# Performance work log

Measured on AMD Instinct MI355X. Metric: run time of the kernel, lower is better.

Reference implementation:

```python
import jax, jax.numpy as jnp
import numpy as np

HEAD = 4
EPS = 1e-12


def _l2norm(x, axis):
    # torch F.normalize: x / max(||x||_2, eps)
    return x / jnp.maximum(jnp.linalg.norm(x, axis=axis, keepdims=True), EPS)


def setup_inputs() -> dict:
    key = jax.random.key(0)
    ks = jax.random.split(key, 12)
    n, t, c, h, w = 2, 7, 96, 96, 96
    inp = {
        "curr_feat": jax.random.normal(ks[0], (n, c, h, w), jnp.float32),
        "index_feat_set_s1": jax.random.normal(ks[1], (n, t, c, h, w), jnp.float32),
        "anchor_feat": jax.random.normal(ks[2], (n, c, h, w), jnp.float32),
        "sparse_feat_set_s1": jax.random.normal(ks[3], (n, t, c, h, w), jnp.float32),
        "sparse_feat_set_s2": jax.random.normal(ks[4], (n, t, c, h, w), jnp.float32),
        "sparse_feat_set_s3": jax.random.normal(ks[5], (n, t, c, h, w), jnp.float32),
        # absolute pixel coordinates (x,y interleaved per frame), mostly in-bounds
        # with a little overshoot to exercise zeros padding of grid_sample
        "location_feat": jax.random.uniform(ks[6], (n, t * 2, h, w), jnp.float32, minval=-2.0, maxval=float(w) + 1.0),
        "proj_w": 0.02 * jax.random.normal(ks[7], (c, c), jnp.float32),
        "proj_b": jnp.zeros((c,), jnp.float32),
        "fusion_w": 0.02 * jax.random.normal(ks[8], (c, 3 * c), jnp.float32),
        "fusion_b": jnp.zeros((c,), jnp.float32),
    }
    return inp


def reference(curr_feat, index_feat_set_s1, anchor_feat, sparse_feat_set_s1,
              sparse_feat_set_s2, sparse_feat_set_s3, location_feat,
              proj_w, proj_b, fusion_w, fusion_b):
    n, c, h, w = anchor_feat.shape
    t = sparse_feat_set_s1.shape[1]
    hd = c // HEAD
    hw = h * w

    # ---- flow-guided nearest grid_sample (align_corners=True, zeros pad) ----
    loc = location_feat.reshape(n, t, 2, h, w)  # (n,t,2,h,w): [x, y] pixel coords
    gx = 2.0 * loc[:, :, 0] / max(w - 1, 1) - 1.0
    gy = 2.0 * loc[:, :, 1] / max(h - 1, 1) - 1.0
    ix = jnp.round((gx + 1.0) * 0.5 * (w - 1))  # nearest (round-half-even, as torch)
    iy = jnp.round((gy + 1.0) * 0.5 * (h - 1))
    valid = (ix >= 0) & (ix <= w - 1) & (iy >= 0) & (iy <= h - 1)
    lin = (jnp.clip(iy, 0, h - 1).astype(jnp.int32) * w
           + jnp.clip(ix, 0, w - 1).astype(jnp.int32)).reshape(n, t, 1, hw)
    vmask = valid.reshape(n, t, 1, hw)

    def sample(f):  # f: (n,t,c,h,w) -> gathered (n,t,c,hw)
        g = jnp.take_along_axis(f.reshape(n, t, c, hw), lin, axis=3)
        return jnp.where(vmask, g, 0.0)

    samp1 = sample(sparse_feat_set_s1)
    samp2 = sample(sparse_feat_set_s2)
    samp3 = sample(sparse_feat_set_s3)
    sampi = sample(index_feat_set_s1)

    # ---- per-pixel multi-head max-correlation over t frames ----
    # queries: normalize over full channel dim c BEFORE splitting into heads
    q = _l2norm(curr_feat.reshape(n, c, hw).transpose(0, 2, 1), -1).reshape(n, hw, HEAD, hd)
    k = _l2norm(sampi.transpose(0, 3, 1, 2), -1).reshape(n, hw, t, HEAD, hd)
    scores = jnp.einsum('npthd,nphd->npht', k, q)  # scale == 1.0 in mode='max'
    corr_soft = jnp.max(scores, axis=3)     # (n,hw,head)
    corr_index = jnp.argmax(scores, axis=3)  # (n,hw,head), first-max like torch

    soft_img = jnp.broadcast_to(corr_soft[..., None], (n, hw, HEAD, hd)) \
                  .reshape(n, h, w, c).transpose(0, 3, 1, 2)  # (n,c,h,w)
    idx = jnp.broadcast_to(corr_index[..., None], (n, hw, HEAD, hd)) \
             .reshape(n, hw, c).transpose(0, 2, 1)[:, None]  # (n,1,c,hw)

    def pick(samp):  # select winning frame per (channel-group, pixel)
        return jnp.take_along_axis(samp, idx, axis=1)[:, 0].reshape(n, c, h, w)

    cat = jnp.concatenate([pick(samp1), pick(samp2), pick(samp3)], axis=1)  # (n,3c,h,w)
    out = jnp.einsum('ndhw,cd->nchw', cat, fusion_w) + fusion_b[None, :, None, None]
    out = out * soft_img
    out = jnp.einsum('nchw,dc->ndhw', out, proj_w) + proj_b[None, :, None, None]
    return out + anchor_feat
```

## Files before the change

kernel.cpp:

```cpp
#include <hip/hip_runtime.h>
#include <hip/hip_bf16.h>

#define N_    2
#define T_    7
#define C_    96
#define H_    96
#define W_    96
#define HW_   9216
#define HEAD_ 4
#define HD_   24
#define C3_   288
#define P_    16
#define QP_   100
#define CATP_ 292
#define NBLK_ (N_ * (HW_ / P_))
#define PLANES_ 14
#define CHUNK_  48
#define NCHUNK_ 192
#define TBLK_ (PLANES_ * NCHUNK_)

typedef unsigned int u32;

__device__ __forceinline__ float bits2f(u32 b) {
    union { u32 u; float f; } x; x.u = b; return x.f;
}

__device__ __forceinline__ unsigned short f2bf(float f) {
    union { __hip_bfloat16 h; unsigned short s; } u;
    u.h = __float2bfloat16(f);
    return u.s;
}

template<bool BF16>
__device__ __forceinline__ float ld1(const void* p, int i) {
    if constexpr (BF16) return bits2f(((u32)((const unsigned short*)p)[i]) << 16);
    else                return ((const float*)p)[i];
}

template<bool BF16>
__device__ __forceinline__ void ld4w(const void* p, int i, float w[4]) {
    if constexpr (BF16) {
        const uint2 u = ((const uint2*)p)[i >> 2];
        w[0] = bits2f(u.x << 16);
        w[1] = bits2f(u.x & 0xFFFF0000u);
        w[2] = bits2f(u.y << 16);
        w[3] = bits2f(u.y & 0xFFFF0000u);
    } else {
        const float4 v = *((const float4*)((const float*)p + i));
        w[0] = v.x; w[1] = v.y; w[2] = v.z; w[3] = v.w;
    }
}

template<bool BF16>
__device__ __forceinline__ void st1(void* p, int i, float v) {
    if constexpr (BF16) ((unsigned short*)p)[i] = f2bf(v);
    else                ((float*)p)[i] = v;
}

template<bool BF16>
__device__ __forceinline__ void st4w(void* p, int i, const float v[4]) {
    if constexpr (BF16) {
        uint2 w;
        w.x = (u32)f2bf(v[0]) | ((u32)f2bf(v[1]) << 16);
        w.y = (u32)f2bf(v[2]) | ((u32)f2bf(v[3]) << 16);
        ((uint2*)p)[i >> 2] = w;
    } else {
        *((float4*)((float*)p + i)) = make_float4(v[0], v[1], v[2], v[3]);
    }
}

__device__ __forceinline__ bool block_detect_bf16(const u32* __restrict__ w,
                                                  int tid, int* s_flag) {
    if (tid < 64) {
        u32 x = w[tid];
        u32 f = x & 0x7FFFu;
        int inwin = (f >= 0x3A00u) && (f <= 0x4200u);
        unsigned long long m = __ballot(inwin);
        if (tid == 0) *s_flag = (__popcll(m) >= 40) ? 1 : 0;
    }
    __syncthreads();
    return *s_flag != 0;
}

template<bool BF16>
__device__ __forceinline__ void transp_swz(const void* __restrict__ src,
                                           void* __restrict__ dst,
                                           int pl, int x0, int tid, char* raw) {
    if constexpr (BF16) {
        unsigned short* tile = (unsigned short*)raw;
        const unsigned short* s = (const unsigned short*)src;
        unsigned short* d = (unsigned short*)dst;
        for (int i = tid; i < C_ * (CHUNK_ / 4); i += 256) {
            int ch = i / 12, xq = i - ch * 12;
            const ushort4 v = *((const ushort4*)(s + (pl * C_ + ch) * HW_ + x0 + 4 * xq));
            int g = (ch >> 2) ^ (xq & 7);
            int chl = ch & 3;
            tile[(4 * xq + 0) * 96 + 4 * g + chl] = v.x;
            tile[(4 * xq + 1) * 96 + 4 * g + chl] = v.y;
            tile[(4 * xq + 2) * 96 + 4 * g + chl] = v.z;
            tile[(4 * xq + 3) * 96 + 4 * g + chl] = v.w;
        }
        __syncthreads();
        for (int i = tid; i < CHUNK_ * (C_ / 4); i += 256) {
            int p = i / 24, cq = i - p * 24;
            int g = cq ^ ((p >> 2) & 7);
            const ushort4 v = *((const ushort4*)&tile[p * 96 + 4 * g]);
            *((ushort4*)(d + (pl * HW_ + x0 + p) * C_ + 4 * cq)) = v;
        }
    } else {
        float* tile = (float*)raw;
        const float* s = (const float*)src;
        float* d = (float*)dst;
        for (int i = tid; i < C_ * (CHUNK_ / 4); i += 256) {
            int ch = i / 12, xq = i - ch * 12;
            const float4 v = *((const float4*)(s + (pl * C_ + ch) * HW_ + x0 + 4 * xq));
            int g = (ch >> 2) ^ (xq & 7);
            int chl = ch & 3;
            tile[(4 * xq + 0) * 96 + 4 * g + chl] = v.x;
            tile[(4 * xq + 1) * 96 + 4 * g + chl] = v.y;
            tile[(4 * xq + 2) * 96 + 4 * g + chl] = v.z;
            tile[(4 * xq + 3) * 96 + 4 * g + chl] = v.w;
        }
        __syncthreads();
        for (int i = tid; i < CHUNK_ * (C_ / 4); i += 256) {
            int p = i / 24, cq = i - p * 24;
            int g = cq ^ ((p >> 2) & 7);
            const float4 v = *((const float4*)&tile[p * 96 + 4 * g]);
            *((float4*)(d + (pl * HW_ + x0 + p) * C_ + 4 * cq)) = v;
        }
    }
}

__global__ __launch_bounds__(256) void transp_kernel(
    const void* __restrict__ a0, const void* __restrict__ a1,
    const void* __restrict__ a2, const void* __restrict__ a3,
    void* __restrict__ dstb, unsigned long long szb,
    const u32* __restrict__ detect_src)
{
    __shared__ __align__(16) char raw[CHUNK_ * 96 * 4];
    __shared__ int s_flag;
    const int arr = blockIdx.y;
    const void* src = (arr == 0) ? a0 : (arr == 1) ? a1 : (arr == 2) ? a2 : a3;
    void* dst = (char*)dstb + (unsigned long long)arr * szb;
    const int tid = threadIdx.x;
    const int pl = blockIdx.x / NCHUNK_;
    const int x0 = (blockIdx.x - pl * NCHUNK_) * CHUNK_;
    const bool bf = block_detect_bf16(detect_src, tid, &s_flag);
    if (bf) transp_swz<true >(src, dst, pl, x0, tid, raw);
    else    transp_swz<false>(src, dst, pl, x0, tid, raw);
}

template<bool BF16, bool TGB>
__device__ __forceinline__ void argmax_body(
    const void* __restrict__ curr, const void* __restrict__ loc,
    const void* __restrict__ kT,
    float* __restrict__ ws_best, int* __restrict__ ws_gbase,
    float* s_u, int (*s_lin)[P_], float (*s_red)[8],
    float (*s_best)[HEAD_], int (*s_bidx)[HEAD_], float* s_inv)
{
#define S_Q(pp, ch)  s_u[(pp) * QP_ + (ch)]
#define S_K(pp, ch)  s_u[P_ * QP_ + (pp) * QP_ + (ch)]
    const int tid = threadIdx.x;
    const int b  = blockIdx.x;
    const int nn = b / (HW_ / P_);
    const int p0 = (b - nn * (HW_ / P_)) * P_;

    if (tid < T_ * P_) {
        int t = tid / P_, pp = tid - t * P_;
        int p = p0 + pp;
        float x = ld1<BF16>(loc, (nn * 2 * T_ + 2 * t    ) * HW_ + p);
        float y = ld1<BF16>(loc, (nn * 2 * T_ + 2 * t + 1) * HW_ + p);
        float gx = 2.0f * x / 95.0f - 1.0f;
        float gy = 2.0f * y / 95.0f - 1.0f;
        float fx = (gx + 1.0f) * 0.5f * 95.0f;
        float fy = (gy + 1.0f) * 0.5f * 95.0f;
        float ix = rintf(fx), iy = rintf(fy);
        bool v = (ix >= 0.0f) && (ix <= 95.0f) && (iy >= 0.0f) && (iy <= 95.0f);
        s_lin[t][pp] = v ? ((int)iy * W_ + (int)ix) : -1;
    }
    if (tid >= 128 && tid < 128 + P_ * HEAD_) {
        int q = tid - 128;
        s_best[q >> 2][q & 3] = -3.0e38f; s_bidx[q >> 2][q & 3] = 0;
    }

    for (int i = tid; i < C_ * (P_ / 4); i += 256) {
        int ch = i >> 2, pq = i & 3;
        float w[4];
        ld4w<BF16>(curr, (nn * C_ + ch) * HW_ + p0 + 4 * pq, w);
        S_Q(4 * pq + 0, ch) = w[0]; S_Q(4 * pq + 1, ch) = w[1];
        S_Q(4 * pq + 2, ch) = w[2]; S_Q(4 * pq + 3, ch) = w[3];
    }
    __syncthreads();

    if (tid < P_ * 8) {
        int pp = tid >> 3, j = tid & 7;
        float s = 0.f;
        #pragma unroll
        for (int k = 0; k < 12; ++k) { float v = S_Q(pp, j * 12 + k); s += v * v; }
        s_red[pp][j] = s;
    }
    __syncthreads();
    if (tid < P_) {
        float s = 0.f;
        #pragma unroll
        for (int j = 0; j < 8; ++j) s += s_red[tid][j];
        s_inv[tid] = 1.0f / fmaxf(sqrtf(s), 1e-12f);
    }
    __syncthreads();
    for (int i = tid; i < C_ * P_; i += 256) {
        int pp = i & (P_ - 1), ch = i >> 4;
        S_Q(pp, ch) *= s_inv[pp];
    }

    const int pp0 = tid / 24,        j0 = tid - pp0 * 24;
    const int pp1 = (tid + 256) / 24, j1 = (tid + 256) - pp1 * 24;
    const bool has1 = (tid < 128);

    float4 ka0, ka1;
    {
        int lin = s_lin[0][pp0];
        float w[4] = {0.f, 0.f, 0.f, 0.f};
        if (lin >= 0) ld4w<BF16>(kT, ((nn * T_) * HW_ + lin) * C_ + 4 * j0, w);
        ka0 = make_float4(w[0], w[1], w[2], w[3]);
        if (has1) {
            int lin2 = s_lin[0][pp1];
            float w2[4] = {0.f, 0.f, 0.f, 0.f};
            if (lin2 >= 0) ld4w<BF16>(kT, ((nn * T_) * HW_ + lin2) * C_ + 4 * j1, w2);
            ka1 = make_float4(w2[0], w2[1], w2[2], w2[3]);
        }
    }

    for (int t = 0; t < T_; ++t) {
        __syncthreads();
        *((float4*)&S_K(pp0, 4 * j0)) = ka0;
        if (has1) *((float4*)&S_K(pp1, 4 * j1)) = ka1;
        if (t + 1 < T_) {
            int lin = s_lin[t + 1][pp0];
            float w[4] = {0.f, 0.f, 0.f, 0.f};
            if (lin >= 0) ld4w<BF16>(kT, ((nn * T_ + t + 1) * HW_ + lin) * C_ + 4 * j0, w);
            ka0 = make_float4(w[0], w[1], w[2], w[3]);
            if (has1) {
                int lin2 = s_lin[t + 1][pp1];
                float w2[4] = {0.f, 0.f, 0.f, 0.f};
                if (lin2 >= 0) ld4w<BF16>(kT, ((nn * T_ + t + 1) * HW_ + lin2) * C_ + 4 * j1, w2);
                ka1 = make_float4(w2[0], w2[1], w2[2], w2[3]);
            }
        }
        __syncthreads();
        if (tid < P_ * 8) {
            int pp = tid >> 3, j = tid & 7;
            float s = 0.f;
            #pragma unroll
            for (int k = 0; k < 12; ++k) { float v = S_K(pp, j * 12 + k); s += v * v; }
            s_red[pp][j] = s;
        }
        __syncthreads();
        if (tid < P_) {
            float s = 0.f;
            #pragma unroll
            for (int j = 0; j < 8; ++j) s += s_red[tid][j];
            s_inv[tid] = 1.0f / fmaxf(sqrtf(s), 1e-12f);
        }
        __syncthreads();
        if (tid < P_ * HEAD_) {
            int pp = tid >> 2, h = tid & 3;
            float s = 0.f;
            #pragma unroll
            for (int dq = 0; dq < 6; ++dq) {
                const float4 kv = *((const float4*)&S_K(pp, h * HD_ + 4 * dq));
                const float4 qv = *((const float4*)&S_Q(pp, h * HD_ + 4 * dq));
                s += kv.x * qv.x; s += kv.y * qv.y; s += kv.z * qv.z; s += kv.w * qv.w;
            }
            s *= s_inv[pp];
            if (s > s_best[pp][h]) { s_best[pp][h] = s; s_bidx[pp][h] = t; }
        }
    }
    if (tid < P_ * HEAD_) {
        int pp = tid >> 2, h = tid & 3;
        int bt = s_bidx[pp][h];
        int lin = s_lin[bt][pp];
        int g = (nn * HW_ + p0 + pp) * HEAD_ + h;
        ws_best[g] = s_best[pp][h];
        int gb;
        if (lin < 0)       gb = -1;
        else if (TGB)      gb = ((nn * T_ + bt) * HW_ + lin) * C_;
        else               gb = (nn * T_ + bt) * C_ * HW_ + lin;
        ws_gbase[g] = gb;
    }
#undef S_Q
#undef S_K
}

template<bool TGB>
__global__ __launch_bounds__(256, 8) void argmax_kernel(
    const void* __restrict__ curr, const void* __restrict__ loc,
    const void* __restrict__ kT,
    float* __restrict__ ws_best, int* __restrict__ ws_gbase)
{
    __shared__ __align__(16) float s_u[2 * P_ * QP_];
    __shared__ int   s_lin[T_][P_];
    __shared__ float s_red[P_][8];
    __shared__ float s_best[P_][HEAD_];
    __shared__ int   s_bidx[P_][HEAD_];
    __shared__ float s_inv[P_];
    __shared__ int   s_flag;
    const bool bf = block_detect_bf16((const u32*)curr, threadIdx.x, &s_flag);
    if (bf) argmax_body<true , TGB>(curr, loc, kT, ws_best, ws_gbase, s_u, s_lin, s_red, s_best, s_bidx, s_inv);
    else    argmax_body<false, TGB>(curr, loc, kT, ws_best, ws_gbase, s_u, s_lin, s_red, s_best, s_bidx, s_inv);
}

__global__ __launch_bounds__(256, 8) void fused_kernel(
    const void* __restrict__ curr, const void* __restrict__ loc,
    const void* __restrict__ kT,
    const void* __restrict__ s1, const void* __restrict__ s2,
    const void* __restrict__ s3,
    void* __restrict__ s123T, unsigned long long szb,
    float* __restrict__ ws_best, int* __restrict__ ws_gbase)
{
    __shared__ __align__(16) char raw[CHUNK_ * 96 * 4];
    __shared__ int s_flag;
    const int tid = threadIdx.x;
    const bool bf = block_detect_bf16((const u32*)curr, tid, &s_flag);
    const int bx = blockIdx.x;
    if (bx < NBLK_) {
        float* s_u            = (float*)raw;
        int   (*s_lin)[P_]    = (int(*)[P_])   (raw + 12800);
        float (*s_red)[8]     = (float(*)[8])  (raw + 13248);
        float (*s_best)[HEAD_]= (float(*)[HEAD_])(raw + 13760);
        int   (*s_bidx)[HEAD_]= (int(*)[HEAD_]) (raw + 14016);
        float* s_inv          = (float*)(raw + 14272);
        if (bf) argmax_body<true , true>(curr, loc, kT, ws_best, ws_gbase,
                                         s_u, s_lin, s_red, s_best, s_bidx, s_inv);
        else    argmax_body<false, true>(curr, loc, kT, ws_best, ws_gbase,
                                         s_u, s_lin, s_red, s_best, s_bidx, s_inv);
    } else {
        int t = bx - NBLK_;
        int arr = t / TBLK_;
        int bxx = t - arr * TBLK_;
        const void* src = (arr == 0) ? s1 : (arr == 1) ? s2 : s3;
        void* dst = (char*)s123T + (unsigned long long)arr * szb;
        int pl = bxx / NCHUNK_;
        int x0 = (bxx - pl * NCHUNK_) * CHUNK_;
        if (bf) transp_swz<true >(src, dst, pl, x0, tid, raw);
        else    transp_swz<false>(src, dst, pl, x0, tid, raw);
    }
}

template<bool BF16, bool TRANS>
__device__ __forceinline__ void catgemv_body(
    const void* __restrict__ anchor, const void* __restrict__ s1,
    const void* __restrict__ s2, const void* __restrict__ s3,
    const void* __restrict__ pw, const void* __restrict__ pb,
    const void* __restrict__ fw, const void* __restrict__ fb,
    void* __restrict__ outp,
    const float* __restrict__ ws_best, const int* __restrict__ ws_gbase,
    float* s_u, float (*s_mid)[QP_], float (*s_best)[HEAD_], int (*s_gbase)[HEAD_])
{
#define S_CAT(pp, d) s_u[(pp) * CATP_ + (d)]
    const int tid = threadIdx.x;
    const int b  = blockIdx.x;
    const int nn = b / (HW_ / P_);
    const int p0 = (b - nn * (HW_ / P_)) * P_;

    if (tid < P_ * HEAD_) {
        int pp = tid >> 2, h = tid & 3;
        int g = (nn * HW_ + p0 + pp) * HEAD_ + h;
        s_best[pp][h]  = ws_best[g];
        s_gbase[pp][h] = ws_gbase[g];
    }
    __syncthreads();

    if constexpr (TRANS) {
        for (int i = tid; i < P_ * 72; i += 256) {
            int px = i / 72, j = i - px * 72;
            int set = j / 24, jj = j - set * 24;
            int gb = s_gbase[px][jj / 6];
            float w[4] = {0.f, 0.f, 0.f, 0.f};
            if (gb >= 0) {
                const void* sp = (set == 0) ? s1 : (set == 1) ? s2 : s3;
                ld4w<BF16>(sp, gb + 4 * jj, w);
            }
            *((float4*)&S_CAT(px, set * C_ + 4 * jj)) = make_float4(w[0], w[1], w[2], w[3]);
        }
    } else {
        for (int i = tid; i < C3_ * P_; i += 256) {
            int pp = i / C3_, d = i - pp * C3_;
            int set = d / C_, ch = d - set * C_;
            int gb = s_gbase[pp][ch / HD_];
            float v = 0.f;
            if (gb >= 0) {
                const void* sp = (set == 0) ? s1 : (set == 1) ? s2 : s3;
                v = ld1<BF16>(sp, gb + ch * HW_);
            }
            S_CAT(pp, d) = v;
        }
    }
    __syncthreads();

    if (tid < 192) {
        const int cp = tid >> 2, pq = tid & 3;
        const int co0 = cp * 2, px0 = pq * 4;
        float acc[2][4];
        #pragma unroll
        for (int r = 0; r < 2; ++r)
            #pragma unroll
            for (int k = 0; k < 4; ++k) acc[r][k] = 0.f;
        for (int d = 0; d < C3_; d += 4) {
            float4 cv[4];
            #pragma unroll
            for (int k = 0; k < 4; ++k) cv[k] = *((const float4*)&S_CAT(px0 + k, d));
            #pragma unroll
            for (int r = 0; r < 2; ++r) {
                float w[4]; ld4w<BF16>(fw, (co0 + r) * C3_ + d, w);
                #pragma unroll
                for (int k = 0; k < 4; ++k)
                    acc[r][k] += w[0] * cv[k].x + w[1] * cv[k].y + w[2] * cv[k].z + w[3] * cv[k].w;
            }
        }
        const int hh = co0 / HD_;
        #pragma unroll
        for (int r = 0; r < 2; ++r) {
            float fbv = ld1<BF16>(fb, co0 + r);
            #pragma unroll
            for (int k = 0; k < 4; ++k)
                s_mid[px0 + k][co0 + r] = (acc[r][k] + fbv) * s_best[px0 + k][hh];
        }
    }
    __syncthreads();

    if (tid < 192) {
        const int dp = tid >> 2, pq = tid & 3;
        const int do0 = dp * 2, px0 = pq * 4;
        float acc[2][4];
        #pragma unroll
        for (int r = 0; r < 2; ++r)
            #pragma unroll
            for (int k = 0; k < 4; ++k) acc[r][k] = 0.f;
        for (int c = 0; c < C_; c += 4) {
            float4 mv[4];
            #pragma unroll
            for (int k = 0; k < 4; ++k) mv[k] = *((const float4*)&s_mid[px0 + k][c]);
            #pragma unroll
            for (int r = 0; r < 2; ++r) {
                float w[4]; ld4w<BF16>(pw, (do0 + r) * C_ + c, w);
                #pragma unroll
                for (int k = 0; k < 4; ++k)
                    acc[r][k] += w[0] * mv[k].x + w[1] * mv[k].y + w[2] * mv[k].z + w[3] * mv[k].w;
            }
        }
        #pragma unroll
        for (int r = 0; r < 2; ++r) {
            float pbv = ld1<BF16>(pb, do0 + r);
            float av[4];
            ld4w<BF16>(anchor, (nn * C_ + do0 + r) * HW_ + p0 + px0, av);
            float res[4];
            #pragma unroll
            for (int k = 0; k < 4; ++k) res[k] = acc[r][k] + pbv + av[k];
            st4w<BF16>(outp, (nn * C_ + do0 + r) * HW_ + p0 + px0, res);
        }
    }
#undef S_CAT
}

template<bool TRANS>
__global__ __launch_bounds__(256, 6) void catgemv_kernel(
    const void* __restrict__ curr, const void* __restrict__ anchor,
    const void* __restrict__ s1, const void* __restrict__ s2,
    const void* __restrict__ s3, const void* __restrict__ pw,
    const void* __restrict__ pb, const void* __restrict__ fw,
    const void* __restrict__ fb, void* __restrict__ outp,
    const float* __restrict__ ws_best, const int* __restrict__ ws_gbase)
{
    __shared__ __align__(16) float s_u[P_ * CATP_];
    __shared__ __align__(16) float s_mid[P_][QP_];
    __shared__ float s_best[P_][HEAD_];
    __shared__ int   s_gbase[P_][HEAD_];
    __shared__ int   s_flag;
    const bool bf = block_detect_bf16((const u32*)curr, threadIdx.x, &s_flag);
    if (bf) catgemv_body<true , TRANS>(anchor, s1, s2, s3, pw, pb, fw, fb, outp, ws_best, ws_gbase,
                                       s_u, s_mid, s_best, s_gbase);
    else    catgemv_body<false, TRANS>(anchor, s1, s2, s3, pw, pb, fw, fb, outp, ws_best, ws_gbase,
                                       s_u, s_mid, s_best, s_gbase);
}

template<bool BF16>
__device__ __forceinline__ void mono_body(
    const void* __restrict__ curr, const void* __restrict__ idxf,
    const void* __restrict__ anchor, const void* __restrict__ s1,
    const void* __restrict__ s2, const void* __restrict__ s3,
    const void* __restrict__ loc, const void* __restrict__ pw,
    const void* __restrict__ pb, const void* __restrict__ fw,
    const void* __restrict__ fb, void* __restrict__ outp,
    float* s_u, float (*s_mid)[QP_], int (*s_lin)[P_], float (*s_red)[8],
    float (*s_best)[HEAD_], int (*s_bidx)[HEAD_], float* s_inv)
{
#define S_Q(pp, ch)  s_u[(pp) * QP_ + (ch)]
#define S_K(pp, ch)  s_u[P_ * QP_ + (pp) * QP_ + (ch)]
#define S_CAT(pp, d) s_u[(pp) * CATP_ + (d)]
    const int tid = threadIdx.x;
    const int b  = blockIdx.x;
    const int nn = b / (HW_ / P_);
    const int p0 = (b - nn * (HW_ / P_)) * P_;

    if (tid < T_ * P_) {
        int t = tid / P_, pp = tid - t * P_;
        int p = p0 + pp;
        float x = ld1<BF16>(loc, (nn * 2 * T_ + 2 * t    ) * HW_ + p);
        float y = ld1<BF16>(loc, (nn * 2 * T_ + 2 * t + 1) * HW_ + p);
        float gx = 2.0f * x / 95.0f - 1.0f;
        float gy = 2.0f * y / 95.0f - 1.0f;
        float fx = (gx + 1.0f) * 0.5f * 95.0f;
        float fy = (gy + 1.0f) * 0.5f * 95.0f;
        float ix = rintf(fx), iy = rintf(fy);
        bool v = (ix >= 0.0f) && (ix <= 95.0f) && (iy >= 0.0f) && (iy <= 95.0f);
        s_lin[t][pp] = v ? ((int)iy * W_ + (int)ix) : -1;
    }
    if (tid >= 128 && tid < 128 + P_ * HEAD_) {
        int q = tid - 128;
        s_best[q >> 2][q & 3] = -3.0e38f; s_bidx[q >> 2][q & 3] = 0;
    }
    for (int i = tid; i < C_ * (P_ / 4); i += 256) {
        int ch = i >> 2, pq = i & 3;
        float w[4];
        ld4w<BF16>(curr, (nn * C_ + ch) * HW_ + p0 + 4 * pq, w);
        S_Q(4 * pq + 0, ch) = w[0]; S_Q(4 * pq + 1, ch) = w[1];
        S_Q(4 * pq + 2, ch) = w[2]; S_Q(4 * pq + 3, ch) = w[3];
    }
    __syncthreads();
    if (tid < P_ * 8) {
        int pp = tid >> 3, j = tid & 7;
        float s = 0.f;
        #pragma unroll
        for (int k = 0; k < 12; ++k) { float v = S_Q(pp, j * 12 + k); s += v * v; }
        s_red[pp][j] = s;
    }
    __syncthreads();
    if (tid < P_) {
        float s = 0.f;
        #pragma unroll
        for (int j = 0; j < 8; ++j) s += s_red[tid][j];
        s_inv[tid] = 1.0f / fmaxf(sqrtf(s), 1e-12f);
    }
    __syncthreads();
    for (int i = tid; i < C_ * P_; i += 256) {
        int pp = i & (P_ - 1), ch = i >> 4;
        S_Q(pp, ch) *= s_inv[pp];
    }
    for (int t = 0; t < T_; ++t) {
        __syncthreads();
        for (int i = tid; i < C_ * P_; i += 256) {
            int ch = i / P_, pp = i - ch * P_;
            int lin = s_lin[t][pp];
            S_K(pp, ch) = (lin >= 0) ? ld1<BF16>(idxf, ((nn * T_ + t) * C_ + ch) * HW_ + lin) : 0.0f;
        }
        __syncthreads();
        if (tid < P_ * 8) {
            int pp = tid >> 3, j = tid & 7;
            float s = 0.f;
            #pragma unroll
            for (int k = 0; k < 12; ++k) { float v = S_K(pp, j * 12 + k); s += v * v; }
            s_red[pp][j] = s;
        }
        __syncthreads();
        if (tid < P_) {
            float s = 0.f;
            #pragma unroll
            for (int j = 0; j < 8; ++j) s += s_red[tid][j];
            s_inv[tid] = 1.0f / fmaxf(sqrtf(s), 1e-12f);
        }
        __syncthreads();
        if (tid < P_ * HEAD_) {
            int pp = tid >> 2, h = tid & 3;
            float s = 0.f;
            #pragma unroll
            for (int dq = 0; dq < 6; ++dq) {
                const float4 kv = *((const float4*)&S_K(pp, h * HD_ + 4 * dq));
                const float4 qv = *((const float4*)&S_Q(pp, h * HD_ + 4 * dq));
                s += kv.x * qv.x; s += kv.y * qv.y; s += kv.z * qv.z; s += kv.w * qv.w;
            }
            s *= s_inv[pp];
            if (s > s_best[pp][h]) { s_best[pp][h] = s; s_bidx[pp][h] = t; }
        }
    }
    __syncthreads();
    for (int i = tid; i < C3_ * P_; i += 256) {
        int pp = i / C3_, d = i - pp * C3_;
        int set = d / C_, ch = d - set * C_;
        int h = ch / HD_;
        int bt = s_bidx[pp][h];
        int lin = s_lin[bt][pp];
        float v = 0.f;
        if (lin >= 0) {
            const void* sp = (set == 0) ? s1 : (set == 1) ? s2 : s3;
            v = ld1<BF16>(sp, ((nn * T_ + bt) * C_ + ch) * HW_ + lin);
        }
        S_CAT(pp, d) = v;
    }
    __syncthreads();
    if (tid < 96) {
        const int cq = tid >> 2, pq = tid & 3;
        const int co0 = cq * 4, px0 = pq * 4;
        float acc[4][4];
        #pragma unroll
        for (int r = 0; r < 4; ++r)
            #pragma unroll
            for (int k = 0; k < 4; ++k) acc[r][k] = 0.f;
        for (int d = 0; d < C3_; d += 4) {
            float4 cv[4];
            #pragma unroll
            for (int k = 0; k < 4; ++k) cv[k] = *((const float4*)&S_CAT(px0 + k, d));
            #pragma unroll
            for (int r = 0; r < 4; ++r) {
                float w[4]; ld4w<BF16>(fw, (co0 + r) * C3_ + d, w);
                #pragma unroll
                for (int k = 0; k < 4; ++k)
                    acc[r][k] += w[0] * cv[k].x + w[1] * cv[k].y + w[2] * cv[k].z + w[3] * cv[k].w;
            }
        }
        const int hh = co0 / HD_;
        #pragma unroll
        for (int r = 0; r < 4; ++r) {
            float fbv = ld1<BF16>(fb, co0 + r);
            #pragma unroll
            for (int k = 0; k < 4; ++k)
                s_mid[px0 + k][co0 + r] = (acc[r][k] + fbv) * s_best[px0 + k][hh];
        }
    }
    __syncthreads();
    if (tid < 96) {
        const int dq = tid >> 2, pq = tid & 3;
        const int do0 = dq * 4, px0 = pq * 4;
        float acc[4][4];
        #pragma unroll
        for (int r = 0; r < 4; ++r)
            #pragma unroll
            for (int k = 0; k < 4; ++k) acc[r][k] = 0.f;
        for (int c = 0; c < C_; c += 4) {
            float4 mv[4];
            #pragma unroll
            for (int k = 0; k < 4; ++k) mv[k] = *((const float4*)&s_mid[px0 + k][c]);
            #pragma unroll
            for (int r = 0; r < 4; ++r) {
                float w[4]; ld4w<BF16>(pw, (do0 + r) * C_ + c, w);
                #pragma unroll
                for (int k = 0; k < 4; ++k)
                    acc[r][k] += w[0] * mv[k].x + w[1] * mv[k].y + w[2] * mv[k].z + w[3] * mv[k].w;
            }
        }
        #pragma unroll
        for (int r = 0; r < 4; ++r) {
            float pbv = ld1<BF16>(pb, do0 + r);
            float av[4];
            ld4w<BF16>(anchor, (nn * C_ + do0 + r) * HW_ + p0 + px0, av);
            float res[4];
            #pragma unroll
            for (int k = 0; k < 4; ++k) res[k] = acc[r][k] + pbv + av[k];
            st4w<BF16>(outp, (nn * C_ + do0 + r) * HW_ + p0 + px0, res);
        }
    }
#undef S_Q
#undef S_K
#undef S_CAT
}

__global__ __launch_bounds__(256) void mono_kernel(
    const void* __restrict__ curr, const void* __restrict__ idxf,
    const void* __restrict__ anchor, const void* __restrict__ s1,
    const void* __restrict__ s2, const void* __restrict__ s3,
    const void* __restrict__ loc, const void* __restrict__ pw,
    const void* __restrict__ pb, const void* __restrict__ fw,
    const void* __restrict__ fb, void* __restrict__ outp)
{
    __shared__ __align__(16) float s_u[P_ * CATP_];
    __shared__ __align__(16) float s_mid[P_][QP_];
    __shared__ int   s_lin[T_][P_];
    __shared__ float s_red[P_][8];
    __shared__ float s_best[P_][HEAD_];
    __shared__ int   s_bidx[P_][HEAD_];
    __shared__ float s_inv[P_];
    __shared__ int   s_flag;
    const bool bf = block_detect_bf16((const u32*)curr, threadIdx.x, &s_flag);
    if (bf) mono_body<true >(curr, idxf, anchor, s1, s2, s3, loc, pw, pb, fw, fb, outp,
                             s_u, s_mid, s_lin, s_red, s_best, s_bidx, s_inv);
    else    mono_body<false>(curr, idxf, anchor, s1, s2, s3, loc, pw, pb, fw, fb, outp,
                             s_u, s_mid, s_lin, s_red, s_best, s_bidx, s_inv);
}

extern "C" void kernel_launch(void* const* d_in, const int* in_sizes, int n_in,
                              void* d_out, int out_size, void* d_ws, size_t ws_size,
                              hipStream_t stream) {
    (void)in_sizes; (void)n_in; (void)out_size;
    const unsigned long long SZB  = (unsigned long long)N_ * T_ * HW_ * C_ * 4ull;
    const unsigned long long AUXB = (unsigned long long)N_ * HW_ * HEAD_ * 4ull;
    char* wsb = (char*)d_ws;

    dim3 grid(NBLK_), block(256);
    if (ws_size >= 4 * SZB + 2 * AUXB) {
        void*  kT       = wsb;
        void*  s123T    = wsb + SZB;
        float* ws_best  = (float*)(wsb + 4 * SZB);
        int*   ws_gbase = (int*)  (wsb + 4 * SZB + AUXB);
        transp_kernel<<<dim3(TBLK_, 1), 256, 0, stream>>>(
            d_in[1], d_in[1], d_in[1], d_in[1], kT, SZB, (const u32*)d_in[0]);
        fused_kernel<<<dim3(NBLK_ + 3 * TBLK_), 256, 0, stream>>>(
            d_in[0], d_in[6], kT, d_in[3], d_in[4], d_in[5], s123T, SZB, ws_best, ws_gbase);
        catgemv_kernel<true><<<grid, block, 0, stream>>>(
            d_in[0], d_in[2],
            (char*)s123T, (char*)s123T + SZB, (char*)s123T + 2 * SZB,
            d_in[7], d_in[8], d_in[9], d_in[10], d_out, ws_best, ws_gbase);
    } else if (ws_size >= SZB + 2 * AUXB) {
        void*  kT       = wsb;
        float* ws_best  = (float*)(wsb + SZB);
        int*   ws_gbase = (int*)  (wsb + SZB + AUXB);
        transp_kernel<<<dim3(TBLK_, 1), 256, 0, stream>>>(
            d_in[1], d_in[1], d_in[1], d_in[1], kT, SZB, (const u32*)d_in[0]);
        argmax_kernel<false><<<grid, block, 0, stream>>>(d_in[0], d_in[6], kT, ws_best, ws_gbase);
        catgemv_kernel<false><<<grid, block, 0, stream>>>(d_in[0], d_in[2], d_in[3], d_in[4], d_in[5],
                                                          d_in[7], d_in[8], d_in[9], d_in[10],
                                                          d_out, ws_best, ws_gbase);
    } else {
        mono_kernel<<<grid, block, 0, stream>>>(d_in[0], d_in[1], d_in[2], d_in[3], d_in[4],
                                                d_in[5], d_in[6], d_in[7], d_in[8], d_in[9],
                                                d_in[10], d_out);
    }
}
```

Baseline: 307.2 us.

## Merge three pipeline kernels into one persistent cooperative kernel with grid syncs

Replaces the transpose, fused argmax/transpose and cat-GEMV launches with a single persistent cooperative kernel of fixed grid size. The kernel loops over work items and uses grid-wide syncs between the phases. This is meant to remove launch gaps and tail effects between the kernels. The transpose chunk width also grows from 48 to 64 pixels, giving bigger tiles and cheaper shift/mask indexing. Risks are grid-sync overhead, the occupancy cap set by the 1536-block grid under 6-block launch bounds, and a fallback to the old multi-kernel path if the cooperative launch fails.

```diff
diff --git a/kernel.cpp b/kernel.cpp
--- a/kernel.cpp
+++ b/kernel.cpp
@@ -1,5 +1,8 @@
 #include <hip/hip_runtime.h>
 #include <hip/hip_bf16.h>
+#include <hip/hip_cooperative_groups.h>
+
+namespace cg = cooperative_groups;
 
 #define N_    2
 #define T_    7
@@ -15,9 +18,11 @@
 #define CATP_ 292
 #define NBLK_ (N_ * (HW_ / P_))
 #define PLANES_ 14
-#define CHUNK_  48
-#define NCHUNK_ 192
+#define CHUNK_  64
+#define NCHUNK_ 144
 #define TBLK_ (PLANES_ * NCHUNK_)
+#define SZB_  49545216ull
+#define COOPG_ 1536
 
 typedef unsigned int u32;
 
@@ -91,7 +96,7 @@
         const unsigned short* s = (const unsigned short*)src;
         unsigned short* d = (unsigned short*)dst;
         for (int i = tid; i < C_ * (CHUNK_ / 4); i += 256) {
-            int ch = i / 12, xq = i - ch * 12;
+            int ch = i >> 4, xq = i & 15;
             const ushort4 v = *((const ushort4*)(s + (pl * C_ + ch) * HW_ + x0 + 4 * xq));
             int g = (ch >> 2) ^ (xq & 7);
             int chl = ch & 3;
@@ -112,7 +117,7 @@
         const float* s = (const float*)src;
         float* d = (float*)dst;
         for (int i = tid; i < C_ * (CHUNK_ / 4); i += 256) {
-            int ch = i / 12, xq = i - ch * 12;
+            int ch = i >> 4, xq = i & 15;
             const float4 v = *((const float4*)(s + (pl * C_ + ch) * HW_ + x0 + 4 * xq));
             int g = (ch >> 2) ^ (xq & 7);
             int chl = ch & 3;
@@ -132,26 +137,22 @@
 }
 
 __global__ __launch_bounds__(256) void transp_kernel(
-    const void* __restrict__ a0, const void* __restrict__ a1,
-    const void* __restrict__ a2, const void* __restrict__ a3,
-    void* __restrict__ dstb, unsigned long long szb,
+    const void* __restrict__ a0, void* __restrict__ dstb,
     const u32* __restrict__ detect_src)
 {
     __shared__ __align__(16) char raw[CHUNK_ * 96 * 4];
     __shared__ int s_flag;
-    const int arr = blockIdx.y;
-    const void* src = (arr == 0) ? a0 : (arr == 1) ? a1 : (arr == 2) ? a2 : a3;
-    void* dst = (char*)dstb + (unsigned long long)arr * szb;
     const int tid = threadIdx.x;
     const int pl = blockIdx.x / NCHUNK_;
     const int x0 = (blockIdx.x - pl * NCHUNK_) * CHUNK_;
     const bool bf = block_detect_bf16(detect_src, tid, &s_flag);
-    if (bf) transp_swz<true >(src, dst, pl, x0, tid, raw);
-    else    transp_swz<false>(src, dst, pl, x0, tid, raw);
+    if (bf) transp_swz<true >(a0, dstb, pl, x0, tid, raw);
+    else    transp_swz<false>(a0, dstb, pl, x0, tid, raw);
 }
 
 template<bool BF16, bool TGB>
 __device__ __forceinline__ void argmax_body(
+    int b,
     const void* __restrict__ curr, const void* __restrict__ loc,
     const void* __restrict__ kT,
     float* __restrict__ ws_best, int* __restrict__ ws_gbase,
@@ -161,7 +162,6 @@
 #define S_Q(pp, ch)  s_u[(pp) * QP_ + (ch)]
 #define S_K(pp, ch)  s_u[P_ * QP_ + (pp) * QP_ + (ch)]
     const int tid = threadIdx.x;
-    const int b  = blockIdx.x;
     const int nn = b / (HW_ / P_);
     const int p0 = (b - nn * (HW_ / P_)) * P_;
 
@@ -212,7 +212,7 @@
         S_Q(pp, ch) *= s_inv[pp];
     }
 
-    const int pp0 = tid / 24,        j0 = tid - pp0 * 24;
+    const int pp0 = tid / 24,         j0 = tid - pp0 * 24;
     const int pp1 = (tid + 256) / 24, j1 = (tid + 256) - pp1 * 24;
     const bool has1 = (tid < 128);
 
@@ -305,16 +305,16 @@
     __shared__ float s_inv[P_];
     __shared__ int   s_flag;
     const bool bf = block_detect_bf16((const u32*)curr, threadIdx.x, &s_flag);
-    if (bf) argmax_body<true , TGB>(curr, loc, kT, ws_best, ws_gbase, s_u, s_lin, s_red, s_best, s_bidx, s_inv);
-    else    argmax_body<false, TGB>(curr, loc, kT, ws_best, ws_gbase, s_u, s_lin, s_red, s_best, s_bidx, s_inv);
-}
-
-__global__ __launch_bounds__(256, 8) void fused_kernel(
+    if (bf) argmax_body<true , TGB>(blockIdx.x, curr, loc, kT, ws_best, ws_gbase, s_u, s_lin, s_red, s_best, s_bidx, s_inv);
+    else    argmax_body<false, TGB>(blockIdx.x, curr, loc, kT, ws_best, ws_gbase, s_u, s_lin, s_red, s_best, s_bidx, s_inv);
+}
+
+__global__ __launch_bounds__(256, 6) void fused_kernel(
     const void* __restrict__ curr, const void* __restrict__ loc,
     const void* __restrict__ kT,
     const void* __restrict__ s1, const void* __restrict__ s2,
     const void* __restrict__ s3,
-    void* __restrict__ s123T, unsigned long long szb,
+    void* __restrict__ s123T,
     float* __restrict__ ws_best, int* __restrict__ ws_gbase)
 {
     __shared__ __align__(16) char raw[CHUNK_ * 96 * 4];
@@ -329,16 +329,16 @@
         float (*s_best)[HEAD_]= (float(*)[HEAD_])(raw + 13760);
         int   (*s_bidx)[HEAD_]= (int(*)[HEAD_]) (raw + 14016);
         float* s_inv          = (float*)(raw + 14272);
-        if (bf) argmax_body<true , true>(curr, loc, kT, ws_best, ws_gbase,
+        if (bf) argmax_body<true , true>(bx, curr, loc, kT, ws_best, ws_gbase,
                                          s_u, s_lin, s_red, s_best, s_bidx, s_inv);
-        else    argmax_body<false, true>(curr, loc, kT, ws_best, ws_gbase,
+        else    argmax_body<false, true>(bx, curr, loc, kT, ws_best, ws_gbase,
                                          s_u, s_lin, s_red, s_best, s_bidx, s_inv);
     } else {
         int t = bx - NBLK_;
         int arr = t / TBLK_;
         int bxx = t - arr * TBLK_;
         const void* src = (arr == 0) ? s1 : (arr == 1) ? s2 : s3;
-        void* dst = (char*)s123T + (unsigned long long)arr * szb;
+        void* dst = (char*)s123T + (unsigned long long)arr * SZB_;
         int pl = bxx / NCHUNK_;
         int x0 = (bxx - pl * NCHUNK_) * CHUNK_;
         if (bf) transp_swz<true >(src, dst, pl, x0, tid, raw);
@@ -348,6 +348,7 @@
 
 template<bool BF16, bool TRANS>
 __device__ __forceinline__ void catgemv_body(
+    int b,
     const void* __restrict__ anchor, const void* __restrict__ s1,
     const void* __restrict__ s2, const void* __restrict__ s3,
     const void* __restrict__ pw, const void* __restrict__ pb,
@@ -358,7 +359,6 @@
 {
 #define S_CAT(pp, d) s_u[(pp) * CATP_ + (d)]
     const int tid = threadIdx.x;
-    const int b  = blockIdx.x;
     const int nn = b / (HW_ / P_);
     const int p0 = (b - nn * (HW_ / P_)) * P_;
 
@@ -477,10 +477,75 @@
     __shared__ int   s_gbase[P_][HEAD_];
     __shared__ int   s_flag;
     const bool bf = block_detect_bf16((const u32*)curr, threadIdx.x, &s_flag);
-    if (bf) catgemv_body<true , TRANS>(anchor, s1, s2, s3, pw, pb, fw, fb, outp, ws_best, ws_gbase,
-                                       s_u, s_mid, s_best, s_gbase);
-    else    catgemv_body<false, TRANS>(anchor, s1, s2, s3, pw, pb, fw, fb, outp, ws_best, ws_gbase,
-                                       s_u, s_mid, s_best, s_gbase);
+    if (bf) catgemv_body<true , TRANS>(blockIdx.x, anchor, s1, s2, s3, pw, pb, fw, fb, outp,
+                                       ws_best, ws_gbase, s_u, s_mid, s_best, s_gbase);
+    else    catgemv_body<false, TRANS>(blockIdx.x, anchor, s1, s2, s3, pw, pb, fw, fb, outp,
+                                       ws_best, ws_gbase, s_u, s_mid, s_best, s_gbase);
+}
+
+__global__ __launch_bounds__(256, 6) void coop_kernel(
+    const void* curr, const void* loc, const void* idxf,
+    const void* s1, const void* s2, const void* s3,
+    const void* anchor, const void* pw, const void* pb,
+    const void* fw, const void* fb, void* outp,
+    void* kT, void* s123T, float* ws_best, int* ws_gbase)
+{
+    __shared__ __align__(16) char raw[25600];
+    __shared__ int s_flag;
+    const int tid = threadIdx.x;
+    const bool bf = block_detect_bf16((const u32*)curr, tid, &s_flag);
+    cg::grid_group grid = cg::this_grid();
+
+    for (unsigned u = blockIdx.x; u < TBLK_; u += gridDim.x) {
+        int pl = u / NCHUNK_;
+        int x0 = (u - pl * NCHUNK_) * CHUNK_;
+        if (bf) transp_swz<true >(idxf, kT, pl, x0, tid, raw);
+        else    transp_swz<false>(idxf, kT, pl, x0, tid, raw);
+        __syncthreads();
+    }
+    grid.sync();
+
+    for (unsigned u = blockIdx.x; u < NBLK_ + 3 * TBLK_; u += gridDim.x) {
+        if (u < NBLK_) {
+            float* s_u            = (float*)raw;
+            int   (*s_lin)[P_]    = (int(*)[P_])   (raw + 12800);
+            float (*s_best)[HEAD_]= (float(*)[HEAD_])(raw + 13248);
+            int   (*s_bidx)[HEAD_]= (int(*)[HEAD_]) (raw + 13504);
+            float (*s_red)[8]     = (float(*)[8])  (raw + 13760);
+            float* s_inv          = (float*)(raw + 14272);
+            if (bf) argmax_body<true , true>(u, curr, loc, kT, ws_best, ws_gbase,
+                                             s_u, s_lin, s_red, s_best, s_bidx, s_inv);
+            else    argmax_body<false, true>(u, curr, loc, kT, ws_best, ws_gbase,
+                                             s_u, s_lin, s_red, s_best, s_bidx, s_inv);
+        } else {
+            int t = u - NBLK_;
+            int arr = t / TBLK_;
+            int bxx = t - arr * TBLK_;
+            const void* src = (arr == 0) ? s1 : (arr == 1) ? s2 : s3;
+            void* dst = (char*)s123T + (unsigned long long)arr * SZB_;
+            int pl = bxx / NCHUNK_;
+            int x0 = (bxx - pl * NCHUNK_) * CHUNK_;
+            if (bf) transp_swz<true >(src, dst, pl, x0, tid, raw);
+            else    transp_swz<false>(src, dst, pl, x0, tid, raw);
+        }
+        __syncthreads();
+    }
+    grid.sync();
+
+    for (unsigned u = blockIdx.x; u < NBLK_; u += gridDim.x) {
+        float* s_u             = (float*)raw;
+        float (*s_mid)[QP_]    = (float(*)[QP_])(raw + 18688);
+        float (*s_best)[HEAD_] = (float(*)[HEAD_])(raw + 25088);
+        int   (*s_gbase)[HEAD_]= (int(*)[HEAD_]) (raw + 25344);
+        const void* t1 = s123T;
+        const void* t2 = (char*)s123T + SZB_;
+        const void* t3 = (char*)s123T + 2 * SZB_;
+        if (bf) catgemv_body<true , true>(u, anchor, t1, t2, t3, pw, pb, fw, fb, outp,
+                                          ws_best, ws_gbase, s_u, s_mid, s_best, s_gbase);
+        else    catgemv_body<false, true>(u, anchor, t1, t2, t3, pw, pb, fw, fb, outp,
+                                          ws_best, ws_gbase, s_u, s_mid, s_best, s_gbase);
+        __syncthreads();
+    }
 }
 
 template<bool BF16>
@@ -690,7 +755,7 @@
                               void* d_out, int out_size, void* d_ws, size_t ws_size,
                               hipStream_t stream) {
     (void)in_sizes; (void)n_in; (void)out_size;
-    const unsigned long long SZB  = (unsigned long long)N_ * T_ * HW_ * C_ * 4ull;
+    const unsigned long long SZB  = SZB_;
     const unsigned long long AUXB = (unsigned long long)N_ * HW_ * HEAD_ * 4ull;
     char* wsb = (char*)d_ws;
 
@@ -700,20 +765,38 @@
         void*  s123T    = wsb + SZB;
         float* ws_best  = (float*)(wsb + 4 * SZB);
         int*   ws_gbase = (int*)  (wsb + 4 * SZB + AUXB);
-        transp_kernel<<<dim3(TBLK_, 1), 256, 0, stream>>>(
-            d_in[1], d_in[1], d_in[1], d_in[1], kT, SZB, (const u32*)d_in[0]);
-        fused_kernel<<<dim3(NBLK_ + 3 * TBLK_), 256, 0, stream>>>(
-            d_in[0], d_in[6], kT, d_in[3], d_in[4], d_in[5], s123T, SZB, ws_best, ws_gbase);
-        catgemv_kernel<true><<<grid, block, 0, stream>>>(
-            d_in[0], d_in[2],
-            (char*)s123T, (char*)s123T + SZB, (char*)s123T + 2 * SZB,
-            d_in[7], d_in[8], d_in[9], d_in[10], d_out, ws_best, ws_gbase);
+
+        const void* curr = d_in[0]; const void* idxf = d_in[1];
+        const void* anch = d_in[2]; const void* s1i  = d_in[3];
+        const void* s2i  = d_in[4]; const void* s3i  = d_in[5];
+        const void* locp = d_in[6]; const void* pwp  = d_in[7];
+        const void* pbp  = d_in[8]; const void* fwp  = d_in[9];
+        const void* fbp  = d_in[10];
+        void* args[] = {
+            (void*)&curr, (void*)&locp, (void*)&idxf,
+            (void*)&s1i, (void*)&s2i, (void*)&s3i,
+            (void*)&anch, (void*)&pwp, (void*)&pbp,
+            (void*)&fwp, (void*)&fbp, (void*)&d_out,
+            (void*)&kT, (void*)&s123T, (void*)&ws_best, (void*)&ws_gbase
+        };
+        hipError_t err = hipLaunchCooperativeKernel((const void*)coop_kernel,
+                                                    dim3(COOPG_), dim3(256),
+                                                    args, 0, stream);
+        if (err != hipSuccess) {
+            (void)hipGetLastError();
+            transp_kernel<<<dim3(TBLK_), 256, 0, stream>>>(d_in[1], kT, (const u32*)d_in[0]);
+            fused_kernel<<<dim3(NBLK_ + 3 * TBLK_), 256, 0, stream>>>(
+                d_in[0], d_in[6], kT, d_in[3], d_in[4], d_in[5], s123T, ws_best, ws_gbase);
+            catgemv_kernel<true><<<grid, block, 0, stream>>>(
+                d_in[0], d_in[2],
+                (char*)s123T, (char*)s123T + SZB, (char*)s123T + 2 * SZB,
+                d_in[7], d_in[8], d_in[9], d_in[10], d_out, ws_best, ws_gbase);
+        }
     } else if (ws_size >= SZB + 2 * AUXB) {
         void*  kT       = wsb;
         float* ws_best  = (float*)(wsb + SZB);
         int*   ws_gbase = (int*)  (wsb + SZB + AUXB);
-        transp_kernel<<<dim3(TBLK_, 1), 256, 0, stream>>>(
-            d_in[1], d_in[1], d_in[1], d_in[1], kT, SZB, (const u32*)d_in[0]);
+        transp_kernel<<<dim3(TBLK_), 256, 0, stream>>>(d_in[1], kT, (const u32*)d_in[0]);
         argmax_kernel<false><<<grid, block, 0, stream>>>(d_in[0], d_in[6], kT, ws_best, ws_gbase);
         catgemv_kernel<false><<<grid, block, 0, stream>>>(d_in[0], d_in[2], d_in[3], d_in[4], d_in[5],
                                                           d_in[7], d_in[8], d_in[9], d_in[10],
```

Measured after the change: 706.2 us. +129.9%, slower.
